# Kernel optimization log

Measured on AMD Instinct MI355X. Metric: run time of the kernel, lower is better.

## Reference

```python
import jax, jax.numpy as jnp
import numpy as np

D_MODEL = 1024
NUM_HEADS = 16
HEAD_DIM = D_MODEL // NUM_HEADS
B, S = 2, 2048


def setup_inputs() -> dict:
    key = jax.random.key(0)
    ks = jax.random.split(key, 5)
    x = jax.random.normal(ks[0], (B, S, D_MODEL), dtype=jnp.float32)
    # nn.Linear weights are [out_features, in_features]
    Wq = jax.random.normal(ks[1], (D_MODEL, D_MODEL), dtype=jnp.float32) / np.sqrt(D_MODEL)
    Wk = jax.random.normal(ks[2], (HEAD_DIM, D_MODEL), dtype=jnp.float32) / np.sqrt(D_MODEL)
    Wv = jax.random.normal(ks[3], (HEAD_DIM, D_MODEL), dtype=jnp.float32) / np.sqrt(D_MODEL)
    Wo = jax.random.normal(ks[4], (D_MODEL, D_MODEL), dtype=jnp.float32) / np.sqrt(D_MODEL)
    # causal mask, broadcastable to [B, H, S, S]; mask==0 positions get -inf
    mask = jnp.tril(jnp.ones((S, S), dtype=bool))[None, None]
    return {"x": x, "Wq": Wq, "Wk": Wk, "Wv": Wv, "Wo": Wo, "mask": mask}


def reference(x, Wq, Wk, Wv, Wo, mask):
    Bsz, Sl, D = x.shape
    H, hd = NUM_HEADS, HEAD_DIM
    q = (x @ Wq.T).reshape(Bsz, Sl, H, hd)          # [B,S,H,hd]
    k = x @ Wk.T                                    # [B,S,hd] (single shared KV head)
    v = x @ Wv.T                                    # [B,S,hd]
    scale = 1.0 / np.sqrt(hd).astype(np.float32)
    # scores: [B,H,S,S] — full O(n^2) matrix, as in the original module
    scores = jnp.einsum('bshd,btd->bhst', q, k) * scale
    scores = jnp.where(mask, scores, -jnp.inf)
    attn = jax.nn.softmax(scores, axis=-1)
    out = jnp.einsum('bhst,btd->bshd', attn, v).reshape(Bsz, Sl, D)
    return out @ Wo.T
```

## Files before the change

### kernel.cpp

```cpp
#include <hip/hip_runtime.h>
#include <hip/hip_bf16.h>
#include <math.h>

#define BB 2
#define SS 2048
#define DD 1024
#define NH 16
#define HD 64
#define MM (BB * SS)

typedef __hip_bfloat16 bf16;
typedef __bf16 bf16_t;
typedef __attribute__((ext_vector_type(8))) __bf16 bf16x8;
typedef __attribute__((ext_vector_type(4))) __bf16 bf16x4;
typedef __attribute__((ext_vector_type(4))) float floatx4;

__global__ void detect_dtype(const unsigned int* __restrict__ x, int* __restrict__ flag) {
    const int tid = threadIdx.x;
    int good = 0;
    for (int i = tid; i < 256; i += 64) {
        unsigned int bits = (x[i] & 0xFFFFu) << 16;
        float v = __uint_as_float(bits);
        float av = fabsf(v);
        if (av == 0.f || (av >= 9.5367431640625e-7f && av <= 64.f)) good++;
    }
#pragma unroll
    for (int s = 1; s < 64; s <<= 1) good += __shfl_xor(good, s);
    if (tid == 0) *flag = (good >= 240) ? 0 : 1;
}

#define BK 32
#define KP 40

__device__ __forceinline__ bf16x4 cvt4(float4 v) {
    bf16x4 o;
    o[0] = (bf16_t)v.x; o[1] = (bf16_t)v.y; o[2] = (bf16_t)v.z; o[3] = (bf16_t)v.w;
    return o;
}

__global__ __launch_bounds__(256) void proj_qkv(const void* __restrict__ X,
                                                const void* __restrict__ Wq,
                                                const void* __restrict__ Wk,
                                                const void* __restrict__ Wv,
                                                bf16_t* __restrict__ QA,
                                                bf16_t* __restrict__ Kp,
                                                bf16_t* __restrict__ VpT,
                                                const int* __restrict__ flag) {
    const int f = *flag;

    __shared__ bf16_t As[128 * KP];
    __shared__ bf16_t Ws[64 * KP];

    const int tid = threadIdx.x;
    const int wave = tid >> 6, lane = tid & 63;
    const int lo = lane & 15, quad = lane >> 4;
    const int rb = wave * 32;
    const int cb = blockIdx.x;
    const int rowBase = blockIdx.y * 128;

    floatx4 acc[2][4];
#pragma unroll
    for (int i = 0; i < 2; i++)
#pragma unroll
        for (int j = 0; j < 4; j++) acc[i][j] = (floatx4){0.f, 0.f, 0.f, 0.f};

    if (f) {
        const int rA = tid >> 3, sg = tid & 7;
        const float* arow[4];
        const float* wrow[2];
#pragma unroll
        for (int p = 0; p < 4; p++)
            arow[p] = (const float*)X + (size_t)(rowBase + rA + 32 * p) * DD;
#pragma unroll
        for (int p = 0; p < 2; p++) {
            int row = rA + 32 * p;
            if (cb < 16)       wrow[p] = (const float*)Wq + (size_t)(cb * 64 + row) * DD;
            else if (cb == 16) wrow[p] = (const float*)Wk + (size_t)row * DD;
            else               wrow[p] = (const float*)Wv + (size_t)row * DD;
        }
        float4 aR[4], wR[2];
#pragma unroll
        for (int p = 0; p < 4; p++) aR[p] = *(const float4*)(arow[p] + sg * 4);
#pragma unroll
        for (int p = 0; p < 2; p++) wR[p] = *(const float4*)(wrow[p] + sg * 4);

        for (int k0 = 0; k0 < DD; k0 += BK) {
            __syncthreads();
#pragma unroll
            for (int p = 0; p < 4; p++)
                *(bf16x4*)&As[(rA + 32 * p) * KP + sg * 4] = cvt4(aR[p]);
#pragma unroll
            for (int p = 0; p < 2; p++)
                *(bf16x4*)&Ws[(rA + 32 * p) * KP + sg * 4] = cvt4(wR[p]);
            __syncthreads();
            if (k0 + BK < DD) {
#pragma unroll
                for (int p = 0; p < 4; p++) aR[p] = *(const float4*)(arow[p] + k0 + BK + sg * 4);
#pragma unroll
                for (int p = 0; p < 2; p++) wR[p] = *(const float4*)(wrow[p] + k0 + BK + sg * 4);
            }
            bf16x8 afr[2], bfr[4];
#pragma unroll
            for (int i = 0; i < 2; i++)
                afr[i] = *(const bf16x8*)&As[(rb + i * 16 + lo) * KP + quad * 8];
#pragma unroll
            for (int j = 0; j < 4; j++)
                bfr[j] = *(const bf16x8*)&Ws[(j * 16 + lo) * KP + quad * 8];
#pragma unroll
            for (int i = 0; i < 2; i++)
#pragma unroll
                for (int j = 0; j < 4; j++)
                    acc[i][j] = __builtin_amdgcn_mfma_f32_16x16x32_bf16(afr[i], bfr[j], acc[i][j], 0, 0, 0);
        }
    } else {
        const int rA = tid >> 2, sg = tid & 3;
        const bf16_t* arow[2];
        const bf16_t* wrow;
#pragma unroll
        for (int p = 0; p < 2; p++)
            arow[p] = (const bf16_t*)X + (size_t)(rowBase + rA + 64 * p) * DD;
        if (cb < 16)       wrow = (const bf16_t*)Wq + (size_t)(cb * 64 + rA) * DD;
        else if (cb == 16) wrow = (const bf16_t*)Wk + (size_t)rA * DD;
        else               wrow = (const bf16_t*)Wv + (size_t)rA * DD;
        bf16x8 aR[2], wR;
#pragma unroll
        for (int p = 0; p < 2; p++) aR[p] = *(const bf16x8*)(arow[p] + sg * 8);
        wR = *(const bf16x8*)(wrow + sg * 8);

        for (int k0 = 0; k0 < DD; k0 += BK) {
            __syncthreads();
#pragma unroll
            for (int p = 0; p < 2; p++)
                *(bf16x8*)&As[(rA + 64 * p) * KP + sg * 8] = aR[p];
            *(bf16x8*)&Ws[rA * KP + sg * 8] = wR;
            __syncthreads();
            if (k0 + BK < DD) {
#pragma unroll
                for (int p = 0; p < 2; p++) aR[p] = *(const bf16x8*)(arow[p] + k0 + BK + sg * 8);
                wR = *(const bf16x8*)(wrow + k0 + BK + sg * 8);
            }
            bf16x8 afr[2], bfr[4];
#pragma unroll
            for (int i = 0; i < 2; i++)
                afr[i] = *(const bf16x8*)&As[(rb + i * 16 + lo) * KP + quad * 8];
#pragma unroll
            for (int j = 0; j < 4; j++)
                bfr[j] = *(const bf16x8*)&Ws[(j * 16 + lo) * KP + quad * 8];
#pragma unroll
            for (int i = 0; i < 2; i++)
#pragma unroll
                for (int j = 0; j < 4; j++)
                    acc[i][j] = __builtin_amdgcn_mfma_f32_16x16x32_bf16(afr[i], bfr[j], acc[i][j], 0, 0, 0);
        }
    }

#pragma unroll
    for (int i = 0; i < 2; i++)
#pragma unroll
        for (int j = 0; j < 4; j++)
#pragma unroll
            for (int reg = 0; reg < 4; reg++) {
                int row = rowBase + rb + i * 16 + quad * 4 + reg;
                int col = j * 16 + lo;
                bf16_t val = (bf16_t)acc[i][j][reg];
                if (cb < 16)       QA[(size_t)row * DD + cb * 64 + col] = val;
                else if (cb == 16) Kp[(size_t)row * HD + col] = val;
                else               VpT[((size_t)(row >> 11) * HD + col) * SS + (row & (SS - 1))] = val;
            }
}

__global__ __launch_bounds__(256) void proj_o(const bf16_t* __restrict__ AO,
                                              const void* __restrict__ Wo,
                                              void* __restrict__ Cout,
                                              const int* __restrict__ flag) {
    const int f = *flag;

    __shared__ bf16_t As[128 * KP];
    __shared__ bf16_t Ws[64 * KP];

    const int tid = threadIdx.x;
    const int wave = tid >> 6, lane = tid & 63;
    const int lo = lane & 15, quad = lane >> 4;
    const int rb = wave * 32;
    const int colBase = blockIdx.x * 64;
    const int rowBase = blockIdx.y * 128;

    floatx4 acc[2][4];
#pragma unroll
    for (int i = 0; i < 2; i++)
#pragma unroll
        for (int j = 0; j < 4; j++) acc[i][j] = (floatx4){0.f, 0.f, 0.f, 0.f};

    const int rA2 = tid >> 2, sgA = tid & 3;
    const bf16_t* arow[2] = {AO + (size_t)(rowBase + rA2) * DD,
                             AO + (size_t)(rowBase + rA2 + 64) * DD};
    bf16x8 aR[2];
#pragma unroll
    for (int p = 0; p < 2; p++) aR[p] = *(const bf16x8*)(arow[p] + sgA * 8);

    if (f) {
        const int rW = tid >> 3, sgW = tid & 7;
        const float* wrow[2];
#pragma unroll
        for (int p = 0; p < 2; p++)
            wrow[p] = (const float*)Wo + (size_t)(colBase + rW + 32 * p) * DD;
        float4 wR[2];
#pragma unroll
        for (int p = 0; p < 2; p++) wR[p] = *(const float4*)(wrow[p] + sgW * 4);

        for (int k0 = 0; k0 < DD; k0 += BK) {
            __syncthreads();
#pragma unroll
            for (int p = 0; p < 2; p++)
                *(bf16x8*)&As[(rA2 + 64 * p) * KP + sgA * 8] = aR[p];
#pragma unroll
            for (int p = 0; p < 2; p++)
                *(bf16x4*)&Ws[(rW + 32 * p) * KP + sgW * 4] = cvt4(wR[p]);
            __syncthreads();
            if (k0 + BK < DD) {
#pragma unroll
                for (int p = 0; p < 2; p++) aR[p] = *(const bf16x8*)(arow[p] + k0 + BK + sgA * 8);
#pragma unroll
                for (int p = 0; p < 2; p++) wR[p] = *(const float4*)(wrow[p] + k0 + BK + sgW * 4);
            }
            bf16x8 afr[2], bfr[4];
#pragma unroll
            for (int i = 0; i < 2; i++)
                afr[i] = *(const bf16x8*)&As[(rb + i * 16 + lo) * KP + quad * 8];
#pragma unroll
            for (int j = 0; j < 4; j++)
                bfr[j] = *(const bf16x8*)&Ws[(j * 16 + lo) * KP + quad * 8];
#pragma unroll
            for (int i = 0; i < 2; i++)
#pragma unroll
                for (int j = 0; j < 4; j++)
                    acc[i][j] = __builtin_amdgcn_mfma_f32_16x16x32_bf16(afr[i], bfr[j], acc[i][j], 0, 0, 0);
        }
    } else {
        const bf16_t* wrow = (const bf16_t*)Wo + (size_t)(colBase + rA2) * DD;
        bf16x8 wR = *(const bf16x8*)(wrow + sgA * 8);

        for (int k0 = 0; k0 < DD; k0 += BK) {
            __syncthreads();
#pragma unroll
            for (int p = 0; p < 2; p++)
                *(bf16x8*)&As[(rA2 + 64 * p) * KP + sgA * 8] = aR[p];
            *(bf16x8*)&Ws[rA2 * KP + sgA * 8] = wR;
            __syncthreads();
            if (k0 + BK < DD) {
#pragma unroll
                for (int p = 0; p < 2; p++) aR[p] = *(const bf16x8*)(arow[p] + k0 + BK + sgA * 8);
                wR = *(const bf16x8*)(wrow + k0 + BK + sgA * 8);
            }
            bf16x8 afr[2], bfr[4];
#pragma unroll
            for (int i = 0; i < 2; i++)
                afr[i] = *(const bf16x8*)&As[(rb + i * 16 + lo) * KP + quad * 8];
#pragma unroll
            for (int j = 0; j < 4; j++)
                bfr[j] = *(const bf16x8*)&Ws[(j * 16 + lo) * KP + quad * 8];
#pragma unroll
            for (int i = 0; i < 2; i++)
#pragma unroll
                for (int j = 0; j < 4; j++)
                    acc[i][j] = __builtin_amdgcn_mfma_f32_16x16x32_bf16(afr[i], bfr[j], acc[i][j], 0, 0, 0);
        }
    }

#pragma unroll
    for (int i = 0; i < 2; i++)
#pragma unroll
        for (int j = 0; j < 4; j++)
#pragma unroll
            for (int reg = 0; reg < 4; reg++) {
                int row = rowBase + rb + i * 16 + quad * 4 + reg;
                int col = colBase + j * 16 + lo;
                size_t idx = (size_t)row * DD + col;
                if (f) ((float*)Cout)[idx] = acc[i][j][reg];
                else   ((bf16_t*)Cout)[idx] = (bf16_t)acc[i][j][reg];
            }
}

#define PSTR 40
#define ALOG2E 0.18033688011112042f

__global__ __launch_bounds__(512, 4) void attn_mfma(const bf16_t* Q,
                                                    const bf16_t* __restrict__ K,
                                                    const bf16_t* __restrict__ Vt,
                                                    bf16_t* O) {
    const int h = blockIdx.y, b = blockIdx.z;
    const int tid = threadIdx.x;
    const int wq = tid >> 6, lane = tid & 63;
    const int lo = lane & 15, quad = lane >> 4;
    const int x = blockIdx.x;

    const int nA = x + 1;
    int na = 1, bestc = 0x7fffffff;
#pragma unroll
    for (int a = 1; a <= 7; ++a) {
        int cA = (nA + a - 1) / a;
        int cB = (65 - nA + (7 - a)) / (8 - a);
        int c = cA > cB ? cA : cB;
        if (c < bestc) { bestc = c; na = a; }
    }
    int qt, pos, gs;
    if (wq < na) { qt = x;      pos = wq;      gs = na; }
    else         { qt = 63 - x; pos = wq - na; gs = 8 - na; }
    const int q0 = qt * 32;
    const int n = qt + 1;
    const int itS = (n * pos) / gs;
    const int itE = (n * (pos + 1)) / gs;

    __shared__ __align__(16) char smem[4 * 32 * 64 * 4];
    __shared__ float MrgML[4][2][2][16];
    bf16_t* Pw = (bf16_t*)smem + wq * (32 * PSTR);
    float (*MrgO)[32 * 64] = (float (*)[32 * 64])smem;

    bf16x8 qf[2][2];
#pragma unroll
    for (int s = 0; s < 2; s++)
#pragma unroll
        for (int hf = 0; hf < 2; hf++)
            qf[s][hf] = *(const bf16x8*)(Q + ((size_t)(b * SS + q0 + s * 16 + lo)) * DD +
                                         h * HD + hf * 32 + quad * 8);

    floatx4 Oacc[2][4];
    float m_i[2], l_i[2];
#pragma unroll
    for (int s = 0; s < 2; s++) {
#pragma unroll
        for (int dt = 0; dt < 4; dt++) Oacc[s][dt] = (floatx4){0.f, 0.f, 0.f, 0.f};
        m_i[s] = -1e30f; l_i[s] = 0.f;
    }

    const bf16_t* Kb = K + (size_t)b * SS * HD;
    const bf16_t* Vb = Vt + (size_t)b * HD * SS;

    if (itS < itE) {
        bf16x8 kf[2][2];
#pragma unroll
        for (int kt = 0; kt < 2; kt++)
#pragma unroll
            for (int hf = 0; hf < 2; hf++)
                kf[kt][hf] = *(const bf16x8*)(Kb + (size_t)(itS * 32 + kt * 16 + lo) * HD +
                                              hf * 32 + quad * 8);

        for (int it = itS; it < itE; it++) {
            const int t0 = it * 32;

            bf16x8 vf[4];
#pragma unroll
            for (int dt = 0; dt < 4; dt++)
                vf[dt] = *(const bf16x8*)(Vb + (size_t)(dt * 16 + lo) * SS + t0 + quad * 8);

            bf16x8 kn[2][2];
            if (it + 1 < itE) {
#pragma unroll
                for (int kt = 0; kt < 2; kt++)
#pragma unroll
                    for (int hf = 0; hf < 2; hf++)
                        kn[kt][hf] = *(const bf16x8*)(Kb + (size_t)(t0 + 32 + kt * 16 + lo) * HD +
                                                      hf * 32 + quad * 8);
            }

            floatx4 st[2][2];
#pragma unroll
            for (int s = 0; s < 2; s++)
#pragma unroll
                for (int kt = 0; kt < 2; kt++) {
                    floatx4 z = (floatx4){0.f, 0.f, 0.f, 0.f};
                    z = __builtin_amdgcn_mfma_f32_16x16x32_bf16(kf[kt][0], qf[s][0], z, 0, 0, 0);
                    z = __builtin_amdgcn_mfma_f32_16x16x32_bf16(kf[kt][1], qf[s][1], z, 0, 0, 0);
                    st[s][kt] = z;
                }

            if (it == qt) {
#pragma unroll
                for (int s = 0; s < 2; s++) {
                    int q = q0 + s * 16 + lo;
#pragma unroll
                    for (int kt = 0; kt < 2; kt++)
#pragma unroll
                        for (int reg = 0; reg < 4; reg++)
                            if (t0 + kt * 16 + quad * 4 + reg > q) st[s][kt][reg] = -1e30f;
                }
            }

#pragma unroll
            for (int s = 0; s < 2; s++) {
                float mx = fmaxf(fmaxf(fmaxf(st[s][0][0], st[s][0][1]), fmaxf(st[s][0][2], st[s][0][3])),
                                 fmaxf(fmaxf(st[s][1][0], st[s][1][1]), fmaxf(st[s][1][2], st[s][1][3])));
                mx = fmaxf(mx, __shfl_xor(mx, 16));
                mx = fmaxf(mx, __shfl_xor(mx, 32));
                float mn = fmaxf(m_i[s], mx);
                float al = exp2f((m_i[s] - mn) * ALOG2E);
                m_i[s] = mn;
                float mnA = mn * ALOG2E;
                float p[2][4];
#pragma unroll
                for (int kt = 0; kt < 2; kt++)
#pragma unroll
                    for (int reg = 0; reg < 4; reg++)
                        p[kt][reg] = exp2f(st[s][kt][reg] * ALOG2E - mnA);
                float rs = ((p[0][0] + p[0][1]) + (p[0][2] + p[0][3])) +
                           ((p[1][0] + p[1][1]) + (p[1][2] + p[1][3]));
                rs += __shfl_xor(rs, 16);
                rs += __shfl_xor(rs, 32);
                l_i[s] = l_i[s] * al + rs;
#pragma unroll
                for (int kt = 0; kt < 2; kt++) {
                    bf16x4 pk;
#pragma unroll
                    for (int reg = 0; reg < 4; reg++) pk[reg] = (bf16_t)p[kt][reg];
                    *(bf16x4*)&Pw[(s * 16 + lo) * PSTR + kt * 16 + quad * 4] = pk;
                }
#pragma unroll
                for (int dt = 0; dt < 4; dt++) Oacc[s][dt] *= al;
            }

            asm volatile("s_waitcnt lgkmcnt(0)" ::: "memory");

            bf16x8 pb[2];
#pragma unroll
            for (int s = 0; s < 2; s++)
                pb[s] = *(const bf16x8*)&Pw[(s * 16 + lo) * PSTR + quad * 8];
#pragma unroll
            for (int s = 0; s < 2; s++)
#pragma unroll
                for (int dt = 0; dt < 4; dt++)
                    Oacc[s][dt] = __builtin_amdgcn_mfma_f32_16x16x32_bf16(vf[dt], pb[s], Oacc[s][dt], 0, 0, 0);

#pragma unroll
            for (int kt = 0; kt < 2; kt++)
#pragma unroll
                for (int hf = 0; hf < 2; hf++) kf[kt][hf] = kn[kt][hf];
        }
    }

    for (int step = 1; step < 8; step <<= 1) {
        const bool pub = (pos & (2 * step - 1)) == step;
        const bool cmb = ((pos & (2 * step - 1)) == 0) && (pos + step < gs);
        __syncthreads();
        if (pub) {
            float* Ob = MrgO[wq >> 1];
#pragma unroll
            for (int s = 0; s < 2; s++) {
#pragma unroll
                for (int dt = 0; dt < 4; dt++)
#pragma unroll
                    for (int reg = 0; reg < 4; reg++)
                        Ob[(s * 16 + dt * 4 + reg) * 64 + lane] = Oacc[s][dt][reg];
                if (quad == 0) {
                    MrgML[wq >> 1][s][0][lo] = m_i[s];
                    MrgML[wq >> 1][s][1][lo] = l_i[s];
                }
            }
        }
        __syncthreads();
        if (cmb) {
            const int bu = (wq + step) >> 1;
            const float* Ob = MrgO[bu];
#pragma unroll
            for (int s = 0; s < 2; s++) {
                float m1 = MrgML[bu][s][0][lo];
                float l1 = MrgML[bu][s][1][lo];
                float mm = fmaxf(m_i[s], m1);
                float a0 = exp2f((m_i[s] - mm) * ALOG2E);
                float a1 = exp2f((m1 - mm) * ALOG2E);
                m_i[s] = mm;
                l_i[s] = l_i[s] * a0 + l1 * a1;
#pragma unroll
                for (int dt = 0; dt < 4; dt++)
#pragma unroll
                    for (int reg = 0; reg < 4; reg++)
                        Oacc[s][dt][reg] = Oacc[s][dt][reg] * a0 +
                                           Ob[(s * 16 + dt * 4 + reg) * 64 + lane] * a1;
            }
        }
    }

    if (pos == 0) {
#pragma unroll
        for (int s = 0; s < 2; s++) {
            float linv = 1.f / l_i[s];
            bf16_t* Orow = O + ((size_t)(b * SS + q0 + s * 16 + lo)) * DD + h * HD;
#pragma unroll
            for (int dt = 0; dt < 4; dt++) {
                bf16x4 ov;
#pragma unroll
                for (int reg = 0; reg < 4; reg++)
                    ov[reg] = (bf16_t)(Oacc[s][dt][reg] * linv);
                *(bf16x4*)&Orow[dt * 16 + quad * 4] = ov;
            }
        }
    }
}

extern "C" void kernel_launch(void* const* d_in, const int* in_sizes, int n_in,
                              void* d_out, int out_size, void* d_ws, size_t ws_size,
                              hipStream_t stream) {
    const void* x  = d_in[0];
    const void* Wq = d_in[1];
    const void* Wk = d_in[2];
    const void* Wv = d_in[3];
    const void* Wo = d_in[4];

    char* ws = (char*)d_ws;
    int* flag = (int*)ws;
    bf16_t* QA  = (bf16_t*)(ws + 256);
    bf16_t* Kp  = QA + (size_t)MM * DD;
    bf16_t* VpT = Kp + (size_t)MM * HD;

    detect_dtype<<<1, 64, 0, stream>>>((const unsigned int*)x, flag);

    proj_qkv<<<dim3(18, MM / 128), dim3(256), 0, stream>>>(x, Wq, Wk, Wv, QA, Kp, VpT, flag);

    attn_mfma<<<dim3(32, NH, BB), dim3(512), 0, stream>>>(QA, Kp, VpT, QA);

    proj_o<<<dim3(16, MM / 128), dim3(256), 0, stream>>>(QA, Wo, d_out, flag);
}
```

Baseline: 220.8 us.

## Fold softmax scale into Q projection and skip rescales with lazy max update

Multiplies Q by scale*log2(e) when the projection is written, so the attention loop can call exp2 on raw scores without a per-element multiply. The running max is now updated only when some lane's block max exceeds the stored max by more than a threshold of 8 (in log2 units), which skips most O-accumulator rescales and max shuffles. Row sums are kept per lane and reduced across lanes once after the loop rather than every iteration. The trade is a new wave-wide vote branch, plus unnormalized probabilities that can reach 2^8 before the bf16 conversion and accumulation.

```diff
diff --git a/kernel.cpp b/kernel.cpp
--- a/kernel.cpp
+++ b/kernel.cpp
@@ -14,6 +14,8 @@
 typedef __attribute__((ext_vector_type(8))) __bf16 bf16x8;
 typedef __attribute__((ext_vector_type(4))) __bf16 bf16x4;
 typedef __attribute__((ext_vector_type(4))) float floatx4;
+
+#define SCALEQ 0.18033688011112042f
 
 __global__ void detect_dtype(const unsigned int* __restrict__ x, int* __restrict__ flag) {
     const int tid = threadIdx.x;
@@ -162,10 +164,14 @@
             for (int reg = 0; reg < 4; reg++) {
                 int row = rowBase + rb + i * 16 + quad * 4 + reg;
                 int col = j * 16 + lo;
-                bf16_t val = (bf16_t)acc[i][j][reg];
-                if (cb < 16)       QA[(size_t)row * DD + cb * 64 + col] = val;
-                else if (cb == 16) Kp[(size_t)row * HD + col] = val;
-                else               VpT[((size_t)(row >> 11) * HD + col) * SS + (row & (SS - 1))] = val;
+                if (cb < 16) {
+                    QA[(size_t)row * DD + cb * 64 + col] = (bf16_t)(acc[i][j][reg] * SCALEQ);
+                } else if (cb == 16) {
+                    Kp[(size_t)row * HD + col] = (bf16_t)acc[i][j][reg];
+                } else {
+                    VpT[((size_t)(row >> 11) * HD + col) * SS + (row & (SS - 1))] =
+                        (bf16_t)acc[i][j][reg];
+                }
             }
 }
 
@@ -282,7 +288,7 @@
 }
 
 #define PSTR 40
-#define ALOG2E 0.18033688011112042f
+#define DMTHR 8.0f
 
 __global__ __launch_bounds__(512, 4) void attn_mfma(const bf16_t* Q,
                                                     const bf16_t* __restrict__ K,
@@ -325,12 +331,12 @@
                                          h * HD + hf * 32 + quad * 8);
 
     floatx4 Oacc[2][4];
-    float m_i[2], l_i[2];
+    float m_i[2], l_ln[2];
 #pragma unroll
     for (int s = 0; s < 2; s++) {
 #pragma unroll
         for (int dt = 0; dt < 4; dt++) Oacc[s][dt] = (floatx4){0.f, 0.f, 0.f, 0.f};
-        m_i[s] = -1e30f; l_i[s] = 0.f;
+        m_i[s] = -1e30f; l_ln[s] = 0.f;
     }
 
     const bf16_t* Kb = K + (size_t)b * SS * HD;
@@ -388,25 +394,26 @@
 
 #pragma unroll
             for (int s = 0; s < 2; s++) {
-                float mx = fmaxf(fmaxf(fmaxf(st[s][0][0], st[s][0][1]), fmaxf(st[s][0][2], st[s][0][3])),
+                float lm = fmaxf(fmaxf(fmaxf(st[s][0][0], st[s][0][1]), fmaxf(st[s][0][2], st[s][0][3])),
                                  fmaxf(fmaxf(st[s][1][0], st[s][1][1]), fmaxf(st[s][1][2], st[s][1][3])));
-                mx = fmaxf(mx, __shfl_xor(mx, 16));
-                mx = fmaxf(mx, __shfl_xor(mx, 32));
-                float mn = fmaxf(m_i[s], mx);
-                float al = exp2f((m_i[s] - mn) * ALOG2E);
-                m_i[s] = mn;
-                float mnA = mn * ALOG2E;
+                if (__any(lm > m_i[s] + DMTHR)) {
+                    float mx = fmaxf(lm, __shfl_xor(lm, 16));
+                    mx = fmaxf(mx, __shfl_xor(mx, 32));
+                    float mn = fmaxf(m_i[s], mx);
+                    float al = exp2f(m_i[s] - mn);
+                    m_i[s] = mn;
+                    l_ln[s] *= al;
+#pragma unroll
+                    for (int dt = 0; dt < 4; dt++) Oacc[s][dt] *= al;
+                }
                 float p[2][4];
 #pragma unroll
                 for (int kt = 0; kt < 2; kt++)
 #pragma unroll
                     for (int reg = 0; reg < 4; reg++)
-                        p[kt][reg] = exp2f(st[s][kt][reg] * ALOG2E - mnA);
-                float rs = ((p[0][0] + p[0][1]) + (p[0][2] + p[0][3])) +
+                        p[kt][reg] = exp2f(st[s][kt][reg] - m_i[s]);
+                l_ln[s] += ((p[0][0] + p[0][1]) + (p[0][2] + p[0][3])) +
                            ((p[1][0] + p[1][1]) + (p[1][2] + p[1][3]));
-                rs += __shfl_xor(rs, 16);
-                rs += __shfl_xor(rs, 32);
-                l_i[s] = l_i[s] * al + rs;
 #pragma unroll
                 for (int kt = 0; kt < 2; kt++) {
                     bf16x4 pk;
@@ -414,8 +421,6 @@
                     for (int reg = 0; reg < 4; reg++) pk[reg] = (bf16_t)p[kt][reg];
                     *(bf16x4*)&Pw[(s * 16 + lo) * PSTR + kt * 16 + quad * 4] = pk;
                 }
-#pragma unroll
-                for (int dt = 0; dt < 4; dt++) Oacc[s][dt] *= al;
             }
 
             asm volatile("s_waitcnt lgkmcnt(0)" ::: "memory");
@@ -435,6 +440,15 @@
 #pragma unroll
                 for (int hf = 0; hf < 2; hf++) kf[kt][hf] = kn[kt][hf];
         }
+    }
+
+    float l_i[2];
+#pragma unroll
+    for (int s = 0; s < 2; s++) {
+        float l = l_ln[s];
+        l += __shfl_xor(l, 16);
+        l += __shfl_xor(l, 32);
+        l_i[s] = l;
     }
 
     for (int step = 1; step < 8; step <<= 1) {
@@ -465,8 +479,8 @@
                 float m1 = MrgML[bu][s][0][lo];
                 float l1 = MrgML[bu][s][1][lo];
                 float mm = fmaxf(m_i[s], m1);
-                float a0 = exp2f((m_i[s] - mm) * ALOG2E);
-                float a1 = exp2f((m1 - mm) * ALOG2E);
+                float a0 = exp2f(m_i[s] - mm);
+                float a1 = exp2f(m1 - mm);
                 m_i[s] = mm;
                 l_i[s] = l_i[s] * a0 + l1 * a1;
 #pragma unroll
```

New measurement: 219.0 us. Within noise of the previous version (-0.8%).
